# Kernel optimization log

Measured on AMD Instinct MI355X. Metric: run time of the kernel, lower is better.

## Reference

```python
import jax, jax.numpy as jnp
import numpy as np

H, W, P = 480, 600, 2048
N = H * W
_IU = np.triu_indices(4)

def _conv(x, w, b, stride=1):
    y = jax.lax.conv_general_dilated(x, w, (stride, stride), 'SAME',
                                     dimension_numbers=('NCHW', 'OIHW', 'NCHW'))
    return y + b[None, :, None, None]

def _gn(x, scale, bias, groups=16, eps=1e-5):
    n, c, h, w = x.shape
    xg = x.reshape(n, groups, c // groups, h, w)
    mu = xg.mean(axis=(2, 3, 4), keepdims=True)
    var = xg.var(axis=(2, 3, 4), keepdims=True)
    xg = (xg - mu) * jax.lax.rsqrt(var + eps)
    return xg.reshape(n, c, h, w) * scale[None, :, None, None] + bias[None, :, None, None]

def _lrelu(x):
    return jnp.where(x >= 0, x, 0.2 * x)

def setup_inputs():
    key = jax.random.key(0)
    ks = jax.random.split(key, 16)
    def he(k, shape, fan_in):
        return jax.random.normal(k, shape, jnp.float32) * np.float32(np.sqrt(2.0 / fan_in))
    return {
        'depth': jax.random.normal(ks[0], (1, 1, H, W), jnp.float32),
        'pose': jax.random.normal(ks[1], (P, 2, 8), jnp.float32),
        'target_mask': (jax.random.uniform(ks[2], (1, 1, H, W)) > 0.5).astype(jnp.float32),
        'pairs': jax.random.randint(ks[3], (P, 2), 0, N),
        'conv1_w': he(ks[4], (32, 3, 3, 3), 3 * 9), 'conv1_b': jnp.zeros(32),
        'gn1_s': jnp.ones(32), 'gn1_b': jnp.zeros(32),
        'conv2_w': he(ks[5], (64, 32, 3, 3), 32 * 9), 'conv2_b': jnp.zeros(64),
        'gn2_s': jnp.ones(64), 'gn2_b': jnp.zeros(64),
        'conv3_w': he(ks[6], (64, 64, 3, 3), 64 * 9), 'conv3_b': jnp.zeros(64),
        'gn3_s': jnp.ones(64), 'gn3_b': jnp.zeros(64),
        'conv4_w': he(ks[7], (64, 96, 3, 3), 96 * 9), 'conv4_b': jnp.zeros(64),
        'gn4_s': jnp.ones(64), 'gn4_b': jnp.zeros(64),
        'gate_w': he(ks[8], (15, 64), 15), 'gate_b': jnp.zeros(64),
        'hid_w': he(ks[9], (64, 64), 64), 'hid_b': jnp.zeros(64),
        'out_w': he(ks[10], (64, 1), 64), 'out_b': jnp.zeros(1),
    }

def _forward(depth, pose, target_mask, params, pairs):
    (c1w, c1b, g1s, g1b, c2w, c2b, g2s, g2b, c3w, c3b, g3s, g3b,
     c4w, c4b, g4s, g4b, gw, gb, hw_, hb, ow, ob) = params
    idx = pairs[:, 0]
    hh, ww = idx // W, idx % W
    # vectorized replacement of the per-pair python-loop scatter
    attn = jnp.zeros((1, 1, H, W), jnp.float32).at[0, 0, hh, ww].set(1.0)
    std_depth = (depth - depth.mean()) * 10.0
    x = jnp.concatenate([std_depth, target_mask, attn], axis=1)  # [1,3,H,W]
    # res_unet backbone (encoder-decoder, GroupNorm, leaky-relu 0.2)
    c1 = _lrelu(_gn(_conv(x, c1w, c1b), g1s, g1b))               # [1,32,H,W]
    d1 = _lrelu(_gn(_conv(c1, c2w, c2b, stride=2), g2s, g2b))    # [1,64,H/2,W/2]
    bm = _lrelu(_gn(_conv(d1, c3w, c3b), g3s, g3b))              # [1,64,H/2,W/2]
    up = jax.image.resize(bm, (1, 64, H, W), method='nearest')
    u = jnp.concatenate([up, c1], axis=1)                         # [1,96,H,W]
    feats = _lrelu(_gn(_conv(u, c4w, c4b), g4s, g4b))            # [1,64,H,W]
    # vectorized per-pair gather
    fg = feats.reshape(64, N)[:, idx].T                           # [P,64]
    fg = jnp.broadcast_to(fg[:, None, :], (P, 2, 64))
    dg = std_depth.reshape(N)[idx]
    dg = jnp.broadcast_to(dg[:, None, None], (P, 2, 1))
    quat = pose[:, :, :4]
    fingers = pose[:, :, 4:7]
    trans = pose[:, :, 7:8]
    outer = quat[..., :, None] * quat[..., None, :]               # sign-invariant q_i*q_j
    enc = outer[..., _IU[0], _IU[1]]                              # [P,2,10]
    cond = jnp.concatenate([enc, fingers, trans, dg], axis=-1)    # [P,2,15]
    # ContextGate_1d: gated attention over gathered features
    gate = jax.nn.sigmoid(cond @ gw + gb)                         # [P,2,64]
    h = fg * gate
    h = h * jax.lax.rsqrt(jnp.sum(h * h, axis=-1, keepdims=True) + 1e-8)
    h = _lrelu(h @ hw_ + hb)
    return jax.nn.silu(h) @ ow + ob                               # [P,2,1]

def reference(depth, pose, target_mask, pairs, conv1_w, conv1_b, gn1_s, gn1_b,
              conv2_w, conv2_b, gn2_s, gn2_b, conv3_w, conv3_b, gn3_s, gn3_b,
              conv4_w, conv4_b, gn4_s, gn4_b, gate_w, gate_b, hid_w, hid_b,
              out_w, out_b):
    params = (conv1_w, conv1_b, gn1_s, gn1_b, conv2_w, conv2_b, gn2_s, gn2_b,
              conv3_w, conv3_b, gn3_s, gn3_b, conv4_w, conv4_b, gn4_s, gn4_b,
              gate_w, gate_b, hid_w, hid_b, out_w, out_b)
    return _forward(depth, pose, target_mask, params, pairs)
```

## Files before the change

kernel.cpp:

```cpp
#include <hip/hip_runtime.h>
#include <math.h>

#define HH 480
#define WW 600
#define NN (HH*WW)
#define PP 2048
#define H2 240
#define W2 300
#define N2 (H2*W2)

typedef __bf16  bf16x8  __attribute__((ext_vector_type(8)));
typedef float   f32x4   __attribute__((ext_vector_type(4)));
typedef ushort  ushort8 __attribute__((ext_vector_type(8)));

__device__ __forceinline__ ushort f2b(float f) {
    unsigned u = __float_as_uint(f);
    unsigned r = (u + 0x7FFF + ((u >> 16) & 1)) >> 16;
    return (ushort)r;
}

__device__ __forceinline__ bf16x8 ld_bf8(const ushort* p, bool v) {
    ushort8 r = {};
    if (v) r = *(const ushort8*)p;
    return __builtin_bit_cast(bf16x8, r);
}

constexpr size_t alup(size_t x) { return (x + 4095) & ~(size_t)4095; }
constexpr size_t OFF_X   = 4096;
constexpr size_t OFF_FT  = alup(OFF_X   + 3UL*NN*4);
constexpr size_t OFF_C1P = alup(OFF_FT  + 64UL*NN*4);
constexpr size_t OFF_D1R = alup(OFF_C1P + 32UL*NN*2);
constexpr size_t OFF_D1P = alup(OFF_D1R + 64UL*N2*4);
constexpr size_t OFF_BMP = alup(OFF_D1P + 64UL*N2*2);
constexpr size_t OFF_WB2 = alup(OFF_BMP + 64UL*N2*2);
constexpr size_t OFF_WB3 = alup(OFF_WB2 + 36864UL);
constexpr size_t OFF_WB4 = alup(OFF_WB3 + 73728UL);

__global__ void k_sum(const float* __restrict__ d, float* __restrict__ ws) {
    float s = 0.f;
    for (int i = blockIdx.x*blockDim.x + threadIdx.x; i < NN; i += gridDim.x*blockDim.x)
        s += d[i];
    #pragma unroll
    for (int o = 32; o; o >>= 1) s += __shfl_down(s, o, 64);
    __shared__ float sm[4];
    int wid = threadIdx.x >> 6;
    if ((threadIdx.x & 63) == 0) sm[wid] = s;
    __syncthreads();
    if (threadIdx.x == 0) {
        float t = 0.f;
        for (int w = 0; w < (int)(blockDim.x >> 6); ++w) t += sm[w];
        atomicAdd(ws, t);
    }
}

__global__ void k_buildx(const float* __restrict__ depth, const float* __restrict__ mask,
                         const float* __restrict__ ws, float* __restrict__ x) {
    int i = blockIdx.x*blockDim.x + threadIdx.x;
    if (i >= NN) return;
    float mean = ws[0] * (1.0f/NN);
    x[i]        = (depth[i] - mean) * 10.0f;
    x[NN + i]   = mask[i];
    x[2*NN + i] = 0.f;
}

__global__ void k_scatter(const int* __restrict__ pairs, float* __restrict__ x) {
    int p = blockIdx.x*blockDim.x + threadIdx.x;
    if (p < PP) x[2*NN + pairs[2*p]] = 1.0f;
}

__global__ void k_wcvt(const float* __restrict__ w, ushort* __restrict__ dst, int NCH) {
    int e = blockIdx.x*256 + threadIdx.x;
    int total = 9*NCH*64*32;
    if (e >= total) return;
    int k  = e & 31;
    int co = (e >> 5) & 63;
    int rest = e >> 11;
    int c = rest % NCH;
    int t = rest / NCH;
    dst[e] = f2b(w[(co*(NCH*32) + c*32 + k)*9 + t]);
}

template<int CIN, int TCO>
__global__ __launch_bounds__(64) void k_conv1(const float* __restrict__ in,
        const float* __restrict__ w, const float* __restrict__ bias,
        float* __restrict__ out) {
    int x   = blockIdx.x*64 + threadIdx.x;
    int y   = blockIdx.y;
    int co0 = blockIdx.z*TCO;
    if (x >= WW) return;
    float acc[TCO];
    #pragma unroll
    for (int c = 0; c < TCO; ++c) acc[c] = bias[co0+c];
    int  xb   = x - 1;
    bool xint = (xb >= 0) && (xb + 2 < WW);
    for (int ci = 0; ci < CIN; ++ci) {
        const float* ip = in + (long)ci*NN;
        float iv[3][3];
        #pragma unroll
        for (int dy = 0; dy < 3; ++dy) {
            int iy = y + dy - 1;
            if ((unsigned)iy < (unsigned)HH) {
                const float* rp = ip + (long)iy*WW + xb;
                if (xint) { iv[dy][0]=rp[0]; iv[dy][1]=rp[1]; iv[dy][2]=rp[2]; }
                else {
                    #pragma unroll
                    for (int dx = 0; dx < 3; ++dx) {
                        int ix = xb + dx;
                        iv[dy][dx] = ((unsigned)ix < (unsigned)WW) ? ip[(long)iy*WW+ix] : 0.f;
                    }
                }
            } else iv[dy][0]=iv[dy][1]=iv[dy][2]=0.f;
        }
        const float* wp = w + ((long)co0*CIN + ci)*9;
        #pragma unroll
        for (int c = 0; c < TCO; ++c)
            #pragma unroll
            for (int k = 0; k < 9; ++k)
                acc[c] += iv[k/3][k%3] * wp[(long)c*CIN*9 + k];
    }
    float* op = out + (size_t)(y*WW + x)*32 + co0;
    #pragma unroll
    for (int c = 0; c < TCO; ++c) op[c] = acc[c];
}

__global__ __launch_bounds__(256) void k_gnstats_pk(const float* __restrict__ x,
        float* __restrict__ stat, int npx) {
    int o = threadIdx.x & 3;
    float s[8], s2[8];
    #pragma unroll
    for (int j = 0; j < 8; ++j) { s[j] = 0.f; s2[j] = 0.f; }
    for (int e = blockIdx.x*256 + threadIdx.x; e < npx*4; e += gridDim.x*256) {
        int px = e >> 2;
        const float* p = x + (size_t)px*32 + o*8;
        #pragma unroll
        for (int j = 0; j < 8; ++j) { float v = p[j]; s[j] += v; s2[j] += v*v; }
    }
    float gs[4], gs2[4];
    #pragma unroll
    for (int j = 0; j < 4; ++j) { gs[j] = s[2*j]+s[2*j+1]; gs2[j] = s2[2*j]+s2[2*j+1]; }
    #pragma unroll
    for (int off = 4; off < 64; off <<= 1)
        #pragma unroll
        for (int j = 0; j < 4; ++j) {
            gs[j]  += __shfl_xor(gs[j],  off, 64);
            gs2[j] += __shfl_xor(gs2[j], off, 64);
        }
    __shared__ float sm[4][4][8];
    int wv = threadIdx.x >> 6;
    if ((threadIdx.x & 63) < 4) {
        #pragma unroll
        for (int j = 0; j < 4; ++j) { sm[wv][o][j] = gs[j]; sm[wv][o][4+j] = gs2[j]; }
    }
    __syncthreads();
    if (threadIdx.x < 32) {
        int o2 = threadIdx.x >> 3, k = threadIdx.x & 7;
        float t = sm[0][o2][k] + sm[1][o2][k] + sm[2][o2][k] + sm[3][o2][k];
        int g = o2*4 + (k & 3);
        atomicAdd(&stat[(k >> 2)*16 + g], t);
    }
}

template<int CH, int CHPER>
__global__ void k_gnpack(const float* __restrict__ x, ushort* __restrict__ y,
                         const float* __restrict__ scale, const float* __restrict__ bias,
                         const float* __restrict__ stat, int npx) {
    constexpr int PARTS = CH/16;
    int e = blockIdx.x*256 + threadIdx.x;
    if (e >= npx*PARTS) return;
    int px   = e / PARTS;
    int part = e - px*PARTS;
    const float* p = x + (size_t)px*CH + part*16;
    ushort*      q = y + (size_t)px*CH + part*16;
    float cnt = (float)CHPER * (float)npx;
    #pragma unroll
    for (int j = 0; j < 16; ++j) {
        int c = part*16 + j;
        int g = c / CHPER;
        float mu  = stat[g] / cnt;
        float var = stat[16+g] / cnt - mu*mu;
        float rs  = rsqrtf(var + 1e-5f);
        float v = (p[j] - mu) * rs * scale[c] + bias[c];
        q[j] = f2b(v >= 0.f ? v : 0.2f*v);
    }
}

template<int MODE>
__global__ __launch_bounds__(256) void k_mconv(const ushort* __restrict__ inA,
        const ushort* __restrict__ inB, const ushort* __restrict__ wb,
        const float* __restrict__ bias, float* __restrict__ out,
        float* __restrict__ stat) {
    constexpr int Ho  = (MODE==4) ? HH : H2;
    constexpr int Wo  = (MODE==4) ? WW : W2;
    constexpr int NCH = (MODE==2) ? 1 : (MODE==3) ? 2 : 3;
    __shared__ float sred[4][16][2];

    int w    = threadIdx.x >> 6;
    int lane = threadIdx.x & 63;
    int lm   = lane & 15;
    int lg   = lane >> 4;
    int y0   = blockIdx.y*4;
    int x0   = blockIdx.x*64;
    int y    = y0 + w;

    f32x4 acc[4][4];
    #pragma unroll
    for (int ct = 0; ct < 4; ++ct)
        #pragma unroll
        for (int pt = 0; pt < 4; ++pt) acc[ct][pt] = 0.f;

    #pragma unroll
    for (int kc = 0; kc < NCH; ++kc) {
        #pragma unroll
        for (int t = 0; t < 9; ++t) {
            const int dy = t/3, dx = t - 3*(t/3);
            const ushort* wp = wb + (size_t)((t*NCH + kc)*64)*32;
            bf16x8 a[4];
            #pragma unroll
            for (int ct = 0; ct < 4; ++ct)
                a[ct] = *(const bf16x8*)(wp + (ct*16 + lm)*32 + lg*8);
            int iy = (MODE==2) ? 2*y + dy : y + dy - 1;
            bool rowv = (unsigned)iy < (unsigned)((MODE==3) ? H2 : HH);
            #pragma unroll
            for (int pt = 0; pt < 4; ++pt) {
                int ox = x0 + pt*16 + lm;
                int ix = (MODE==2) ? 2*ox + dx : ox + dx - 1;
                bool v = rowv && ((unsigned)ix < (unsigned)((MODE==3) ? W2 : WW));
                const ushort* bp;
                if (MODE==2) {
                    bp = inA + ((size_t)iy*WW + ix)*32 + lg*8;
                } else if (MODE==3) {
                    bp = inA + ((size_t)iy*W2 + ix)*64 + kc*32 + lg*8;
                } else {
                    bp = (kc < 2) ? inA + ((size_t)(iy>>1)*W2 + (ix>>1))*64 + kc*32 + lg*8
                                  : inB + ((size_t)iy*WW + ix)*32 + lg*8;
                }
                bf16x8 b = ld_bf8(bp, v);
                #pragma unroll
                for (int ct = 0; ct < 4; ++ct)
                    acc[ct][pt] = __builtin_amdgcn_mfma_f32_16x16x32_bf16(a[ct], b, acc[ct][pt], 0, 0, 0);
            }
        }
    }

    #pragma unroll
    for (int ct = 0; ct < 4; ++ct) {
        float s = 0.f, s2 = 0.f;
        #pragma unroll
        for (int pt = 0; pt < 4; ++pt) {
            int pxg = x0 + pt*16 + lm;
            bool vld = pxg < Wo;
            f32x4 r;
            #pragma unroll
            for (int reg = 0; reg < 4; ++reg) {
                int co = ct*16 + lg*4 + reg;
                float v = acc[ct][pt][reg] + bias[co];
                r[reg] = v;
                if (vld) { s += v; s2 += v*v; }
            }
            if (vld)
                *(f32x4*)(out + (size_t)(y*Wo + pxg)*64 + ct*16 + lg*4) = r;
        }
        #pragma unroll
        for (int o = 1; o < 16; o <<= 1) {
            s  += __shfl_xor(s,  o, 64);
            s2 += __shfl_xor(s2, o, 64);
        }
        if (lm == 0) { sred[w][ct*4+lg][0] = s; sred[w][ct*4+lg][1] = s2; }
    }
    __syncthreads();
    if (threadIdx.x < 32) {
        int g = threadIdx.x >> 1, k = threadIdx.x & 1;
        float t = sred[0][g][k] + sred[1][g][k] + sred[2][g][k] + sred[3][g][k];
        atomicAdd(&stat[k*16 + g], t);
    }
}

__global__ void k_mlp(const float* __restrict__ pose, const float* __restrict__ sd,
                      const int* __restrict__ pairs, const float* __restrict__ feats,
                      const float* __restrict__ g4s, const float* __restrict__ g4b,
                      const float* __restrict__ st4,
                      const float* __restrict__ gw, const float* __restrict__ gb,
                      const float* __restrict__ hw, const float* __restrict__ hb,
                      const float* __restrict__ ow, const float* __restrict__ ob,
                      float* __restrict__ out) {
    int wid  = threadIdx.x >> 6;
    int lane = threadIdx.x & 63;
    int t = blockIdx.x*4 + wid;
    int p = t >> 1;
    const float* pp = pose + t*8;
    float q0=pp[0], q1=pp[1], q2=pp[2], q3=pp[3];
    float f0=pp[4], f1=pp[5], f2=pp[6], tr=pp[7];
    int idx = pairs[2*p];
    float dg = sd[idx];
    float cond[15] = {q0*q0,q0*q1,q0*q2,q0*q3,q1*q1,q1*q2,q1*q3,q2*q2,q2*q3,q3*q3,
                      f0,f1,f2,tr,dg};
    float acc = gb[lane];
    #pragma unroll
    for (int k = 0; k < 15; ++k) acc += cond[k]*gw[k*64+lane];
    float gate = 1.f/(1.f+expf(-acc));
    float raw = feats[(size_t)idx*64 + lane];
    int   g4  = lane >> 2;
    float cnt = 4.0f * (float)NN;
    float mu  = st4[g4] / cnt;
    float var = st4[16+g4] / cnt - mu*mu;
    float rs  = rsqrtf(var + 1e-5f);
    float fv  = (raw - mu) * rs * g4s[lane] + g4b[lane];
    float fg  = fv >= 0.f ? fv : 0.2f*fv;
    float h = fg*gate;
    float ss = h*h;
    #pragma unroll
    for (int o = 32; o; o >>= 1) ss += __shfl_xor(ss, o, 64);
    h *= rsqrtf(ss + 1e-8f);
    __shared__ float hs[4][64];
    hs[wid][lane] = h;
    __syncthreads();
    float a2 = hb[lane];
    #pragma unroll 8
    for (int d = 0; d < 64; ++d) a2 += hs[wid][d]*hw[d*64+lane];
    float h2 = a2 >= 0.f ? a2 : 0.2f*a2;
    float si = h2 / (1.f+expf(-h2));
    float v = si * ow[lane];
    #pragma unroll
    for (int o = 32; o; o >>= 1) v += __shfl_xor(v, o, 64);
    if (lane == 0) out[t] = v + ob[0];
}

extern "C" void kernel_launch(void* const* d_in, const int* in_sizes, int n_in,
                              void* d_out, int out_size, void* d_ws, size_t ws_size,
                              hipStream_t stream) {
    const float* depth = (const float*)d_in[0];
    const float* pose  = (const float*)d_in[1];
    const float* mask  = (const float*)d_in[2];
    const int*   pairs = (const int*)  d_in[3];
    const float* c1w = (const float*)d_in[4];  const float* c1b = (const float*)d_in[5];
    const float* g1s = (const float*)d_in[6];  const float* g1b = (const float*)d_in[7];
    const float* c2w = (const float*)d_in[8];  const float* c2b = (const float*)d_in[9];
    const float* g2s = (const float*)d_in[10]; const float* g2b = (const float*)d_in[11];
    const float* c3w = (const float*)d_in[12]; const float* c3b = (const float*)d_in[13];
    const float* g3s = (const float*)d_in[14]; const float* g3b = (const float*)d_in[15];
    const float* c4w = (const float*)d_in[16]; const float* c4b = (const float*)d_in[17];
    const float* g4s = (const float*)d_in[18]; const float* g4b = (const float*)d_in[19];
    const float* gw  = (const float*)d_in[20]; const float* gb  = (const float*)d_in[21];
    const float* hw_ = (const float*)d_in[22]; const float* hb  = (const float*)d_in[23];
    const float* ow  = (const float*)d_in[24]; const float* ob  = (const float*)d_in[25];

    char* base = (char*)d_ws;
    float*  stats = (float*) base;
    float*  X   = (float*) (base + OFF_X);
    float*  FT  = (float*) (base + OFF_FT);
    float*  C1R = FT;
    ushort* C1P = (ushort*)(base + OFF_C1P);
    float*  D1R = (float*) (base + OFF_D1R);
    ushort* D1P = (ushort*)(base + OFF_D1P);
    ushort* BMP = (ushort*)(base + OFF_BMP);
    ushort* WB2 = (ushort*)(base + OFF_WB2);
    ushort* WB3 = (ushort*)(base + OFF_WB3);
    ushort* WB4 = (ushort*)(base + OFF_WB4);
    float* st1 = stats + 16;
    float* st2 = stats + 64;
    float* st3 = stats + 112;
    float* st4 = stats + 160;

    hipMemsetAsync(d_ws, 0, 1024, stream);

    k_sum    <<<1024, 256, 0, stream>>>(depth, stats);
    k_buildx <<<(NN+255)/256, 256, 0, stream>>>(depth, mask, stats, X);
    k_scatter<<<(PP+255)/256, 256, 0, stream>>>(pairs, X);
    k_wcvt   <<< 72, 256, 0, stream>>>(c2w, WB2, 1);
    k_wcvt   <<<144, 256, 0, stream>>>(c3w, WB3, 2);
    k_wcvt   <<<216, 256, 0, stream>>>(c4w, WB4, 3);

    k_conv1<3,16><<<dim3(10, HH, 2), 64, 0, stream>>>(X, c1w, c1b, C1R);
    k_gnstats_pk<<<256, 256, 0, stream>>>(C1R, st1, NN);
    k_gnpack<32,2><<<(NN*2+255)/256, 256, 0, stream>>>(C1R, C1P, g1s, g1b, st1, NN);

    k_mconv<2><<<dim3(5, 60), 256, 0, stream>>>(C1P, nullptr, WB2, c2b, D1R, st2);
    k_gnpack<64,4><<<(N2*4+255)/256, 256, 0, stream>>>(D1R, D1P, g2s, g2b, st2, N2);

    k_mconv<3><<<dim3(5, 60), 256, 0, stream>>>(D1P, nullptr, WB3, c3b, D1R, st3);
    k_gnpack<64,4><<<(N2*4+255)/256, 256, 0, stream>>>(D1R, BMP, g3s, g3b, st3, N2);

    k_mconv<4><<<dim3(10, 120), 256, 0, stream>>>(BMP, C1P, WB4, c4b, FT, st4);

    k_mlp<<<(2*PP)/4, 256, 0, stream>>>(pose, X, pairs, FT, g4s, g4b, st4,
                                        gw, gb, hw_, hb, ow, ob, (float*)d_out);
}
```

Measured before the change: 383.2 us.

## Stage conv input halo tiles in shared memory for MFMA implicit-GEMM convs

The MFMA conv kernels now cooperatively load a row/column halo tile of the input (per 32-channel chunk) into padded LDS, then read the B fragments for all 9 taps from shared memory instead of issuing 9 separate bounds-checked global loads per tap. This lets the overlapping 3x3 windows be reused across taps and rows. For the stride-2 conv2, each block now covers 32 output pixels wide, and the grid is doubled to match. The change adds LDS usage, which may reduce occupancy, and adds block-wide syncs between channel chunks.

```diff
diff --git a/kernel.cpp b/kernel.cpp
--- a/kernel.cpp
+++ b/kernel.cpp
@@ -17,12 +17,6 @@
     unsigned u = __float_as_uint(f);
     unsigned r = (u + 0x7FFF + ((u >> 16) & 1)) >> 16;
     return (ushort)r;
-}
-
-__device__ __forceinline__ bf16x8 ld_bf8(const ushort* p, bool v) {
-    ushort8 r = {};
-    if (v) r = *(const ushort8*)p;
-    return __builtin_bit_cast(bf16x8, r);
 }
 
 constexpr size_t alup(size_t x) { return (x + 4095) & ~(size_t)4095; }
@@ -185,13 +179,20 @@
 }
 
 template<int MODE>
-__global__ __launch_bounds__(256) void k_mconv(const ushort* __restrict__ inA,
+__global__ __launch_bounds__(256) void k_sconv(const ushort* __restrict__ inA,
         const ushort* __restrict__ inB, const ushort* __restrict__ wb,
         const float* __restrict__ bias, float* __restrict__ out,
         float* __restrict__ stat) {
-    constexpr int Ho  = (MODE==4) ? HH : H2;
-    constexpr int Wo  = (MODE==4) ? WW : W2;
-    constexpr int NCH = (MODE==2) ? 1 : (MODE==3) ? 2 : 3;
+    constexpr int Wo   = (MODE==4) ? WW : W2;
+    constexpr int NCH  = (MODE==2) ? 1 : (MODE==3) ? 2 : 3;
+    constexpr int NPT  = (MODE==2) ? 2 : 4;
+    constexpr int ROWS = (MODE==2) ? 9 : 6;
+    constexpr int PXS  = 68;
+    constexpr int CPITCH = 36;
+    constexpr int UNITS = ROWS*PXS*4;
+    constexpr int Hi = (MODE==3) ? H2 : HH;
+    constexpr int Wi = (MODE==3) ? W2 : WW;
+    __shared__ __align__(16) ushort sh[ROWS*PXS*CPITCH];
     __shared__ float sred[4][16][2];
 
     int w    = threadIdx.x >> 6;
@@ -199,17 +200,45 @@
     int lm   = lane & 15;
     int lg   = lane >> 4;
     int y0   = blockIdx.y*4;
-    int x0   = blockIdx.x*64;
+    int x0   = blockIdx.x*(NPT*16);
     int y    = y0 + w;
-
-    f32x4 acc[4][4];
+    int iy0  = (MODE==2) ? 2*y0 : y0 - 1;
+    int ix0  = (MODE==2) ? 2*x0 : x0 - 1;
+
+    f32x4 acc[4][NPT];
     #pragma unroll
     for (int ct = 0; ct < 4; ++ct)
         #pragma unroll
-        for (int pt = 0; pt < 4; ++pt) acc[ct][pt] = 0.f;
+        for (int pt = 0; pt < NPT; ++pt) acc[ct][pt] = 0.f;
+
+    int dsbase = (((MODE==2 ? 2*w*PXS + 2*lm : w*PXS + lm))*CPITCH + lg*8);
 
     #pragma unroll
     for (int kc = 0; kc < NCH; ++kc) {
+        if (kc) __syncthreads();
+        #pragma unroll
+        for (int u0 = 0; u0 < UNITS; u0 += 256) {
+            int u = u0 + threadIdx.x;
+            if (u < UNITS) {
+                int r  = u / (PXS*4);
+                int rm = u - r*(PXS*4);
+                int px = rm >> 2;
+                int q  = rm & 3;
+                int iy = iy0 + r;
+                int ix = ix0 + px;
+                ushort8 val = {};
+                if ((unsigned)iy < (unsigned)Hi && (unsigned)ix < (unsigned)Wi) {
+                    const ushort* sp;
+                    if (MODE==2)      sp = inA + ((size_t)iy*WW + ix)*32 + q*8;
+                    else if (MODE==3) sp = inA + ((size_t)iy*W2 + ix)*64 + kc*32 + q*8;
+                    else if (kc < 2)  sp = inA + ((size_t)(iy>>1)*W2 + (ix>>1))*64 + kc*32 + q*8;
+                    else              sp = inB + ((size_t)iy*WW + ix)*32 + q*8;
+                    val = *(const ushort8*)sp;
+                }
+                *(ushort8*)&sh[(r*PXS + px)*CPITCH + q*8] = val;
+            }
+        }
+        __syncthreads();
         #pragma unroll
         for (int t = 0; t < 9; ++t) {
             const int dy = t/3, dx = t - 3*(t/3);
@@ -218,23 +247,10 @@
             #pragma unroll
             for (int ct = 0; ct < 4; ++ct)
                 a[ct] = *(const bf16x8*)(wp + (ct*16 + lm)*32 + lg*8);
-            int iy = (MODE==2) ? 2*y + dy : y + dy - 1;
-            bool rowv = (unsigned)iy < (unsigned)((MODE==3) ? H2 : HH);
             #pragma unroll
-            for (int pt = 0; pt < 4; ++pt) {
-                int ox = x0 + pt*16 + lm;
-                int ix = (MODE==2) ? 2*ox + dx : ox + dx - 1;
-                bool v = rowv && ((unsigned)ix < (unsigned)((MODE==3) ? W2 : WW));
-                const ushort* bp;
-                if (MODE==2) {
-                    bp = inA + ((size_t)iy*WW + ix)*32 + lg*8;
-                } else if (MODE==3) {
-                    bp = inA + ((size_t)iy*W2 + ix)*64 + kc*32 + lg*8;
-                } else {
-                    bp = (kc < 2) ? inA + ((size_t)(iy>>1)*W2 + (ix>>1))*64 + kc*32 + lg*8
-                                  : inB + ((size_t)iy*WW + ix)*32 + lg*8;
-                }
-                bf16x8 b = ld_bf8(bp, v);
+            for (int pt = 0; pt < NPT; ++pt) {
+                int off = (dy*PXS + (MODE==2 ? pt*32 + dx : pt*16 + dx))*CPITCH;
+                bf16x8 b = *(const bf16x8*)&sh[dsbase + off];
                 #pragma unroll
                 for (int ct = 0; ct < 4; ++ct)
                     acc[ct][pt] = __builtin_amdgcn_mfma_f32_16x16x32_bf16(a[ct], b, acc[ct][pt], 0, 0, 0);
@@ -246,7 +262,7 @@
     for (int ct = 0; ct < 4; ++ct) {
         float s = 0.f, s2 = 0.f;
         #pragma unroll
-        for (int pt = 0; pt < 4; ++pt) {
+        for (int pt = 0; pt < NPT; ++pt) {
             int pxg = x0 + pt*16 + lm;
             bool vld = pxg < Wo;
             f32x4 r;
@@ -374,13 +390,13 @@
     k_gnstats_pk<<<256, 256, 0, stream>>>(C1R, st1, NN);
     k_gnpack<32,2><<<(NN*2+255)/256, 256, 0, stream>>>(C1R, C1P, g1s, g1b, st1, NN);
 
-    k_mconv<2><<<dim3(5, 60), 256, 0, stream>>>(C1P, nullptr, WB2, c2b, D1R, st2);
+    k_sconv<2><<<dim3(10, 60), 256, 0, stream>>>(C1P, nullptr, WB2, c2b, D1R, st2);
     k_gnpack<64,4><<<(N2*4+255)/256, 256, 0, stream>>>(D1R, D1P, g2s, g2b, st2, N2);
 
-    k_mconv<3><<<dim3(5, 60), 256, 0, stream>>>(D1P, nullptr, WB3, c3b, D1R, st3);
+    k_sconv<3><<<dim3(5, 60), 256, 0, stream>>>(D1P, nullptr, WB3, c3b, D1R, st3);
     k_gnpack<64,4><<<(N2*4+255)/256, 256, 0, stream>>>(D1R, BMP, g3s, g3b, st3, N2);
 
-    k_mconv<4><<<dim3(10, 120), 256, 0, stream>>>(BMP, C1P, WB4, c4b, FT, st4);
+    k_sconv<4><<<dim3(10, 120), 256, 0, stream>>>(BMP, C1P, WB4, c4b, FT, st4);
 
     k_mlp<<<(2*PP)/4, 256, 0, stream>>>(pose, X, pairs, FT, g4s, g4b, st4,
                                         gw, gb, hw_, hb, ow, ob, (float*)d_out);
```

Measured after the change: 322.5 us. 1.19x faster.
